# Performance work log

Hardware: AMD Instinct MI355X
Metric: run time of the kernel (lower is better)

The kernel has to match this reference:

```python
import jax, jax.numpy as jnp
import numpy as np

V, L, H, D = 2048, 16, 8, 64   # vocab, max_chars, n_head, word_vec_d
B = 8192                        # number of words in batch (rows of char_code)
NW_TOTAL = 8192                 # len(word_code)
N_NAMES = 2048                  # total names (4 words each)
N_GROUPS = 8                    # groups of names (256 each)
PAD = 0
TEMP = D ** 0.5
LN_EPS = 1e-5


def make_pos():
    freq = D // 2
    inv = 1.0 / np.power(10000.0, np.arange(freq) / freq)
    ph = np.outer(np.arange(L), inv)
    return jnp.asarray(np.hstack([np.cos(ph), np.sin(ph)]).astype(np.float32))


def setup_inputs() -> dict:
    key = jax.random.key(0)
    ks = jax.random.split(key, 8)
    char_emb = jax.random.normal(ks[0], (V, D), jnp.float32) * 0.02
    char_emb = char_emb.at[PAD].set(0.0)  # padding_idx row
    Wc = jax.random.normal(ks[1], (D, 3 * H * D), jnp.float32) * 0.02
    bc = jnp.zeros((3 * H * D,), jnp.float32)
    Wp = jax.random.normal(ks[2], (D, 3 * H * D), jnp.float32) * 0.02
    bp = jnp.zeros((3 * H * D,), jnp.float32)
    gamma = jnp.ones((D,), jnp.float32)
    beta = jnp.zeros((D,), jnp.float32)
    W1 = jax.random.normal(ks[3], (H, 16), jnp.float32) * 0.1
    b1 = jnp.zeros((16,), jnp.float32)
    W2 = jax.random.normal(ks[4], (16, 8), jnp.float32) * 0.1
    b2 = jnp.zeros((8,), jnp.float32)
    char_code = jax.random.randint(ks[5], (B, L), 1, V)
    char_code = char_code.at[::4, -2:].set(PAD)  # some padded tails
    word_code = jax.random.randint(ks[6], (NW_TOTAL,), 0, B)
    n_words = np.full((N_NAMES,), NW_TOTAL // N_NAMES, dtype=np.int64)
    n_names = np.full((N_GROUPS,), N_NAMES // N_GROUPS, dtype=np.int64)
    return {"char_emb": char_emb, "Wc": Wc, "bc": bc, "Wp": Wp, "bp": bp,
            "gamma": gamma, "beta": beta, "W1": W1, "b1": b1, "W2": W2, "b2": b2,
            "char_code": char_code, "word_code": word_code,
            "n_words": n_words, "n_names": n_names}


def reference(char_emb, Wc, bc, Wp, bp, gamma, beta, W1, b1, W2, b2,
              char_code, word_code, n_words, n_names):
    pos = make_pos()
    # ComputeQKV: linear d -> 3*H*d, reshape [N,3,H,D]
    cqkv = (char_emb @ Wc + bc).reshape(V, 3, H, D)
    cq, ck, cv = cqkv[:, 0], cqkv[:, 1], cqkv[:, 2]        # [V,H,D]
    pqkv = (pos @ Wp + bp).reshape(L, 3, H, D)
    pq, pk, pv = pqkv[:, 0], pqkv[:, 1], pqkv[:, 2]        # [L,H,D]
    # precomputed score tables
    char_qk = jnp.einsum('xhd,yhd->hxy', cq, ck).at[:, :, PAD].set(-1e9)  # [H,V,V]
    pos_qk = jnp.einsum('xhd,yhd->hxy', pq, pk)                            # [H,L,L]
    # char_q@pos_k + (pos_q@char_k)^T summed over the first dim of char_pos_qk
    cp = jnp.einsum('vhd,lhd->hvl', cq, pk) + jnp.einsum('lhd,vhd->hvl', pq, ck)  # [H,V,L]
    code = char_code                                        # [B,L]
    # gather-assembled scores, no [H,B*L,V] intermediate
    sim = (char_qk[:, code[:, :, None], code[:, None, :]]   # [H,B,L,L]
           + cp[:, code]
           + pos_qk[:, None]) / TEMP
    attn = jax.nn.softmax(sim, axis=-1)                     # [H,B,L,L] (dropout=0)
    v = jnp.transpose(cv[code], (2, 0, 1, 3)) + pv.transpose(1, 0, 2)[:, None]  # [H,B,L,D]
    out = jnp.einsum('hbij,hbjd->bihd', attn, v)            # [B,L,H,D]
    mu = out.mean(-1, keepdims=True)
    var = out.var(-1, keepdims=True)
    out = (out - mu) / jnp.sqrt(var + LN_EPS) * gamma + beta  # LayerNorm(D)
    char_ft = jnp.transpose(out, (0, 2, 1, 3))              # [B,H,L,D]
    mask = (code != PAD)
    pooled = jnp.einsum('bl,bhld->bhd', mask.astype(out.dtype), char_ft) \
             / mask.sum(-1)[:, None, None]                  # masked mean over chars
    x = jnp.transpose(pooled, (0, 2, 1))                    # [B,D,H]
    x = jax.nn.relu(x @ W1 + b1) @ W2 + b2                  # MLP over head dim -> [B,D,8]
    word_ft = x.reshape(B, -1)[word_code]                   # [NW_TOTAL, D*8]
    nw = np.asarray(n_words)
    seg = jnp.asarray(np.repeat(np.arange(nw.size), nw))
    name_ft = jax.ops.segment_sum(word_ft, seg, num_segments=nw.size) \
              / jnp.asarray(nw, word_ft.dtype)[:, None]     # ragged mean -> [N_NAMES, D*8]
    splits = np.cumsum(np.asarray(n_names))[:-1]
    return tuple(jnp.split(name_ft, splits, axis=0))
```

## Files before the change

### kernel.cpp

```cpp
#include <hip/hip_runtime.h>
#include <hip/hip_bf16.h>
#include <math.h>

typedef __attribute__((ext_vector_type(8))) short bfrag;
typedef __attribute__((ext_vector_type(4))) float ffrag;
typedef __attribute__((ext_vector_type(4))) float f4v;

#define C3 1536
#define PS 24

__device__ __forceinline__ unsigned short f2bf(float f) {
    unsigned u = __float_as_uint(f);
    return (unsigned short)((u + 0x7FFFu + ((u >> 16) & 1u)) >> 16);
}
__device__ __forceinline__ float bf2f(unsigned short s) {
    return __uint_as_float(((unsigned)s) << 16);
}

__device__ __forceinline__ float row16_sum(float x) {
    int v;
    v = __builtin_amdgcn_update_dpp(0, __float_as_int(x), 0xB1, 0xF, 0xF, true);
    x += __int_as_float(v);
    v = __builtin_amdgcn_update_dpp(0, __float_as_int(x), 0x4E, 0xF, 0xF, true);
    x += __int_as_float(v);
    v = __builtin_amdgcn_update_dpp(0, __float_as_int(x), 0x124, 0xF, 0xF, true);
    x += __int_as_float(v);
    v = __builtin_amdgcn_update_dpp(0, __float_as_int(x), 0x128, 0xF, 0xF, true);
    x += __int_as_float(v);
    return x;
}

__global__ __launch_bounds__(256) void precompute_kernel(
    const float* __restrict__ char_emb, const float* __restrict__ Wc, const float* __restrict__ bc,
    const float* __restrict__ Wp, const float* __restrict__ bp,
    unsigned short* __restrict__ cqkv, float* __restrict__ pqkv,
    unsigned short* __restrict__ pbf)
{
    const int b = blockIdx.x;
    const int t = threadIdx.x;
    if (b < 1536) {
        const int mt = b / 6;
        const int nt = b - mt * 6;
        const int m0 = mt * 8;
        const int c = nt * 256 + t;
        const float qs = (c < 512) ? 0.125f : 1.f;
        const float bias = bc[c];
        float acc[8];
        #pragma unroll
        for (int r = 0; r < 8; ++r) acc[r] = bias;
        #pragma unroll 16
        for (int dd = 0; dd < 64; ++dd) {
            const float wv = Wc[dd * C3 + c];
            #pragma unroll
            for (int r = 0; r < 8; ++r)
                acc[r] = fmaf(char_emb[(m0 + r) * 64 + dd], wv, acc[r]);
        }
        #pragma unroll
        for (int r = 0; r < 8; ++r)
            cqkv[(size_t)(m0 + r) * C3 + c] = f2bf(acc[r] * qs);
    } else {
        const int l = b - 1536;
        __shared__ float spos[64];
        if (t < 64) {
            const int f = t & 31;
            const float inv = exp2f(-(float)f * 0.41524101186092034f);
            const float ph = (float)l * inv;
            spos[t] = (t < 32) ? cosf(ph) : sinf(ph);
        }
        __syncthreads();
        #pragma unroll
        for (int cc = 0; cc < 6; ++cc) {
            const int c = t + cc * 256;
            float acc = bp[c];
            #pragma unroll
            for (int dd = 0; dd < 64; ++dd)
                acc = fmaf(spos[dd], Wp[dd * C3 + c], acc);
            pqkv[l * C3 + c] = acc;
            if (c < 1024) {
                const float qs = (c < 512) ? 0.125f : 1.f;
                pbf[(c >> 6) * 1024 + l * 64 + (c & 63)] = f2bf(acc * qs);
            }
        }
    }
}

__global__ __launch_bounds__(256) void vprime_kernel(
    const unsigned short* __restrict__ cqkv, const float* __restrict__ pqkv,
    unsigned short* __restrict__ vtab)
{
    const int c = blockIdx.x;
    const int t = threadIdx.x;
    const int hd8 = t & 63;
    const int l0 = t >> 6;
    const bfrag cv = *(const bfrag*)(cqkv + (size_t)c * C3 + 1024 + hd8 * 8);
    #pragma unroll
    for (int li = 0; li < 4; ++li) {
        const int l = l0 + li * 4;
        const f4v pa = *(const f4v*)(pqkv + l * C3 + 1024 + hd8 * 8);
        const f4v pb = *(const f4v*)(pqkv + l * C3 + 1024 + hd8 * 8 + 4);
        bfrag o;
        #pragma unroll
        for (int j = 0; j < 8; ++j)
            o[j] = (short)f2bf(bf2f((unsigned short)cv[j]) + ((j < 4) ? pa[j] : pb[j - 4]));
        *(bfrag*)(vtab + ((size_t)c * 16 + l) * 512 + hd8 * 8) = o;
    }
}

__global__ __launch_bounds__(256, 8) void attn_kernel(
    const unsigned short* __restrict__ cqkv, const unsigned short* __restrict__ pbf,
    const unsigned short* __restrict__ vtab, const int* __restrict__ char_code,
    const float* __restrict__ gamma, const float* __restrict__ beta,
    float* __restrict__ pooled)
{
    __shared__ __attribute__((aligned(16))) unsigned short sVt[4 * 1024];
    __shared__ __attribute__((aligned(16))) unsigned short sP[4 * 16 * PS];

    const int t = threadIdx.x;
    const int lane = t & 63;
    const int wid = t >> 6;
    const int gw = blockIdx.x * 4 + wid;
    const int w = gw >> 3;
    const int h = gw & 7;
    const int quad = lane >> 4;
    const int n = lane & 15;

    const int code = char_code[w * 16 + n];
    const bool kvalid = (code != 0);
    const unsigned long long msk = __ballot(kvalid);
    const int nv = __popcll(msk & 0xFFFFull);

    float gam[4], bet[4];
    #pragma unroll
    for (int dt = 0; dt < 4; ++dt) {
        gam[dt] = gamma[dt * 16 + n];
        bet[dt] = beta[dt * 16 + n];
    }

    unsigned short* vt = sVt + wid * 1024;
    #pragma unroll
    for (int cc = 0; cc < 2; ++cc) {
        const int d8 = quad + cc * 4;
        const bfrag vb = *(const bfrag*)(vtab + ((size_t)code * 16 + n) * 512 + h * 64 + d8 * 8);
        #pragma unroll
        for (int j = 0; j < 8; ++j) {
            const int d = d8 * 8 + j;
            const int e = ((d >> 4) * 2 + (n >> 3)) * 128
                        + ((d & 15) ^ ((n >> 3) << 2)) * 8 + (n & 7);
            vt[e] = (unsigned short)vb[j];
        }
    }

    ffrag accS = {0.f, 0.f, 0.f, 0.f};
    {
        const unsigned short* cbase = cqkv + (size_t)code * C3 + h * 64;
        const unsigned short* pq = pbf + h * 1024 + n * 64;
        const unsigned short* pk = pbf + (8 + h) * 1024 + n * 64;
        #pragma unroll
        for (int cc = 0; cc < 2; ++cc) {
            const int off = quad * 8 + cc * 32;
            const bfrag cqF = *(const bfrag*)(cbase + off);
            const bfrag ckF = *(const bfrag*)(cbase + 512 + off);
            const bfrag pqF = *(const bfrag*)(pq + off);
            const bfrag pkF = *(const bfrag*)(pk + off);
            accS = __builtin_amdgcn_mfma_f32_16x16x32_bf16(cqF, ckF, accS, 0, 0, 0);
            accS = __builtin_amdgcn_mfma_f32_16x16x32_bf16(cqF, pkF, accS, 0, 0, 0);
            accS = __builtin_amdgcn_mfma_f32_16x16x32_bf16(pqF, pkF, accS, 0, 0, 0);
            accS = __builtin_amdgcn_mfma_f32_16x16x32_bf16(ckF, pqF, accS, 0, 0, 0);
        }
    }

    float pr[4], sm[4];
    #pragma unroll
    for (int r = 0; r < 4; ++r) {
        pr[r] = kvalid ? __expf(accS[r]) : 0.f;
        sm[r] = row16_sum(pr[r]);
    }
    unsigned short* pt = sP + wid * 16 * PS;
    #pragma unroll
    for (int r = 0; r < 4; ++r)
        pt[(quad * 4 + r) * PS + n] = f2bf(pr[r]);

    bfrag ap;
    #pragma unroll
    for (int j = 0; j < 8; ++j) ap[j] = 0;
    if (quad < 2) ap = *(const bfrag*)(pt + n * PS + quad * 8);
    const int q2 = quad & 1;
    ffrag accO[4];
    #pragma unroll
    for (int dt = 0; dt < 4; ++dt) { ffrag z = {0.f,0.f,0.f,0.f}; accO[dt] = z; }
    #pragma unroll
    for (int dt = 0; dt < 4; ++dt) {
        const bfrag bv = *(const bfrag*)(vt + (dt * 2 + q2) * 128 + (n ^ (q2 << 2)) * 8);
        accO[dt] = __builtin_amdgcn_mfma_f32_16x16x32_bf16(ap, bv, accO[dt], 0, 0, 0);
    }

    float ps1[4], ps2[4];
    #pragma unroll
    for (int r = 0; r < 4; ++r) {
        ps1[r] = accO[0][r] + accO[1][r] + accO[2][r] + accO[3][r];
        ps2[r] = accO[0][r]*accO[0][r] + accO[1][r]*accO[1][r]
               + accO[2][r]*accO[2][r] + accO[3][r]*accO[3][r];
        ps1[r] = row16_sum(ps1[r]);
        ps2[r] = row16_sum(ps2[r]);
    }
    float pool[4] = {0.f, 0.f, 0.f, 0.f};
    #pragma unroll
    for (int r = 0; r < 4; ++r) {
        const float mu   = ps1[r] * 0.015625f;
        const float var  = fmaxf(ps2[r] * 0.015625f - mu * mu, 0.f);
        const float rstd = rsqrtf(var + sm[r] * sm[r] * 1e-5f);
        const float iv = ((msk >> (quad * 4 + r)) & 1ull) ? 1.f : 0.f;
        #pragma unroll
        for (int dt = 0; dt < 4; ++dt)
            pool[dt] += iv * fmaf((accO[dt][r] - mu) * rstd, gam[dt], bet[dt]);
    }
    #pragma unroll
    for (int xm = 16; xm <= 32; xm <<= 1) {
        #pragma unroll
        for (int dt = 0; dt < 4; ++dt) pool[dt] += __shfl_xor(pool[dt], xm);
    }
    if (quad == 0) {
        const float invnv = 1.f / (float)nv;
        f4v o;
        #pragma unroll
        for (int dt = 0; dt < 4; ++dt) o[dt] = pool[dt] * invnv;
        *(f4v*)(pooled + (size_t)w * 512 + h * 64 + n * 4) = o;
    }
}

__global__ __launch_bounds__(128) void mlp_avg_kernel(
    const float* __restrict__ pooled, const int* __restrict__ word_code,
    const int* __restrict__ n_words,
    const float* __restrict__ W1, const float* __restrict__ b1,
    const float* __restrict__ W2, const float* __restrict__ b2,
    float* __restrict__ out)
{
    __shared__ float sPool[512];
    __shared__ float sHid[64 * 17];
    __shared__ float sWb[280];
    __shared__ int sred[128];
    const int nm = blockIdx.x;
    const int t = threadIdx.x;
    sWb[t] = W1[t];
    sWb[144 + t] = W2[t];
    if (t < 16) sWb[128 + t] = b1[t];
    if (t < 8)  sWb[272 + t] = b2[t];

    int part = 0;
    for (int i = t; i < nm; i += 128) part += n_words[i];
    sred[t] = part;
    __syncthreads();
    for (int s = 64; s > 0; s >>= 1) {
        if (t < s) sred[t] += sred[t + s];
        __syncthreads();
    }
    const int off = sred[0];
    const int cnt = n_words[nm];

    const int d = t & 63, o4 = (t >> 6) * 4;
    const int dmap = (d & 15) * 4 + (d >> 4);
    float xacc[4] = {0.f, 0.f, 0.f, 0.f};

    for (int r = 0; r < cnt; ++r) {
        const int wc = word_code[off + r];
        __syncthreads();
        *(f4v*)(sPool + t * 4) = *(const f4v*)(pooled + (size_t)wc * 512 + t * 4);
        __syncthreads();
        if (t < 64) {
            float pl[8];
            #pragma unroll
            for (int hh = 0; hh < 8; ++hh) pl[hh] = sPool[hh * 64 + dmap];
            #pragma unroll
            for (int c = 0; c < 16; ++c) {
                float hs = sWb[128 + c];
                #pragma unroll
                for (int hh = 0; hh < 8; ++hh) hs = fmaf(pl[hh], sWb[hh * 16 + c], hs);
                sHid[t * 17 + c] = fmaxf(hs, 0.f);
            }
        }
        __syncthreads();
        #pragma unroll
        for (int c = 0; c < 16; ++c) {
            const float hc = sHid[d * 17 + c];
            #pragma unroll
            for (int oo = 0; oo < 4; ++oo)
                xacc[oo] = fmaf(hc, sWb[144 + c * 8 + o4 + oo], xacc[oo]);
        }
    }
    const float inv = 1.f / (float)cnt;
    f4v res;
    #pragma unroll
    for (int oo = 0; oo < 4; ++oo) res[oo] = xacc[oo] * inv + sWb[272 + o4 + oo];
    *(f4v*)(out + (size_t)nm * 512 + d * 8 + o4) = res;
}

extern "C" void kernel_launch(void* const* d_in, const int* in_sizes, int n_in,
                              void* d_out, int out_size, void* d_ws, size_t ws_size,
                              hipStream_t stream) {
    (void)in_sizes; (void)n_in; (void)out_size; (void)ws_size;
    const float* char_emb = (const float*)d_in[0];
    const float* Wc    = (const float*)d_in[1];
    const float* bc    = (const float*)d_in[2];
    const float* Wp    = (const float*)d_in[3];
    const float* bp    = (const float*)d_in[4];
    const float* gamma = (const float*)d_in[5];
    const float* beta  = (const float*)d_in[6];
    const float* W1    = (const float*)d_in[7];
    const float* b1    = (const float*)d_in[8];
    const float* W2    = (const float*)d_in[9];
    const float* b2    = (const float*)d_in[10];
    const int* char_code = (const int*)d_in[11];
    const int* word_code = (const int*)d_in[12];
    const int* n_words   = (const int*)d_in[13];

    char* ws = (char*)d_ws;
    unsigned short* cqkv = (unsigned short*)ws;
    float* pqkv = (float*)(ws + 6291456);
    unsigned short* pbf  = (unsigned short*)(ws + 6389760);
    unsigned short* vtab = (unsigned short*)(ws + 6422528);
    float* pooled = (float*)(ws + 39976960);
    float* out = (float*)d_out;

    precompute_kernel<<<1552, 256, 0, stream>>>(char_emb, Wc, bc, Wp, bp, cqkv, pqkv, pbf);
    vprime_kernel<<<2048, 256, 0, stream>>>(cqkv, pqkv, vtab);
    attn_kernel<<<16384, 256, 0, stream>>>(cqkv, pbf, vtab, char_code, gamma, beta, pooled);
    mlp_avg_kernel<<<2048, 128, 0, stream>>>(pooled, word_code, n_words,
                                             W1, b1, W2, b2, out);
}
```

Measured before the change: 204.5 us.

## Precompute positional QK scores and fold softmax row sums into an MFMA

The position-only q·k term, which is the same for every word, is now computed once per head in an extra vprime block and loaded as the initial MFMA accumulator. This removes one MFMA per chunk in the attention kernel. The softmax row sum is taken from an MFMA against a ones fragment instead of DPP row reductions. The position-projection precompute is also split across more blocks, and gamma/beta are packed into a table read with vector loads. The changes add small tables and extra blocks, and the row sum now comes from bf16-rounded probabilities.

```diff
diff --git a/kernel.cpp b/kernel.cpp
--- a/kernel.cpp
+++ b/kernel.cpp
@@ -33,8 +33,9 @@
 __global__ __launch_bounds__(256) void precompute_kernel(
     const float* __restrict__ char_emb, const float* __restrict__ Wc, const float* __restrict__ bc,
     const float* __restrict__ Wp, const float* __restrict__ bp,
+    const float* __restrict__ gamma, const float* __restrict__ beta,
     unsigned short* __restrict__ cqkv, float* __restrict__ pqkv,
-    unsigned short* __restrict__ pbf)
+    unsigned short* __restrict__ pbf, float* __restrict__ gbtab)
 {
     const int b = blockIdx.x;
     const int t = threadIdx.x;
@@ -59,7 +60,16 @@
         for (int r = 0; r < 8; ++r)
             cqkv[(size_t)(m0 + r) * C3 + c] = f2bf(acc[r] * qs);
     } else {
-        const int l = b - 1536;
+        const int e = b - 1536;
+        const int l = e / 6;
+        const int cc = e - l * 6;
+        if (b == 1536 && t < 64) {
+            #pragma unroll
+            for (int dt = 0; dt < 4; ++dt) {
+                gbtab[t * 8 + dt]     = gamma[dt * 16 + t];
+                gbtab[t * 8 + 4 + dt] = beta[dt * 16 + t];
+            }
+        }
         __shared__ float spos[64];
         if (t < 64) {
             const int f = t & 31;
@@ -68,28 +78,42 @@
             spos[t] = (t < 32) ? cosf(ph) : sinf(ph);
         }
         __syncthreads();
-        #pragma unroll
-        for (int cc = 0; cc < 6; ++cc) {
-            const int c = t + cc * 256;
-            float acc = bp[c];
-            #pragma unroll
-            for (int dd = 0; dd < 64; ++dd)
-                acc = fmaf(spos[dd], Wp[dd * C3 + c], acc);
-            pqkv[l * C3 + c] = acc;
-            if (c < 1024) {
-                const float qs = (c < 512) ? 0.125f : 1.f;
-                pbf[(c >> 6) * 1024 + l * 64 + (c & 63)] = f2bf(acc * qs);
-            }
+        const int c = t + cc * 256;
+        float acc = bp[c];
+        #pragma unroll
+        for (int dd = 0; dd < 64; ++dd)
+            acc = fmaf(spos[dd], Wp[dd * C3 + c], acc);
+        pqkv[l * C3 + c] = acc;
+        if (c < 1024) {
+            const float qs = (c < 512) ? 0.125f : 1.f;
+            pbf[(c >> 6) * 1024 + l * 64 + (c & 63)] = f2bf(acc * qs);
         }
     }
 }
 
 __global__ __launch_bounds__(256) void vprime_kernel(
     const unsigned short* __restrict__ cqkv, const float* __restrict__ pqkv,
-    unsigned short* __restrict__ vtab)
+    unsigned short* __restrict__ vtab, float* __restrict__ posqk)
 {
     const int c = blockIdx.x;
     const int t = threadIdx.x;
+    if (c >= 2048) {
+        const int h = c - 2048;
+        const int i = t >> 4, j = t & 15;
+        const f4v* qa = (const f4v*)(pqkv + i * C3 + h * 64);
+        const f4v* kb = (const f4v*)(pqkv + j * C3 + 512 + h * 64);
+        float acc = 0.f;
+        #pragma unroll
+        for (int x = 0; x < 16; ++x) {
+            const f4v a = qa[x], bb = kb[x];
+            acc = fmaf(a[0], bb[0], acc);
+            acc = fmaf(a[1], bb[1], acc);
+            acc = fmaf(a[2], bb[2], acc);
+            acc = fmaf(a[3], bb[3], acc);
+        }
+        posqk[h * 256 + (i >> 2) * 64 + j * 4 + (i & 3)] = acc * 0.125f;
+        return;
+    }
     const int hd8 = t & 63;
     const int l0 = t >> 6;
     const bfrag cv = *(const bfrag*)(cqkv + (size_t)c * C3 + 1024 + hd8 * 8);
@@ -109,7 +133,7 @@
 __global__ __launch_bounds__(256, 8) void attn_kernel(
     const unsigned short* __restrict__ cqkv, const unsigned short* __restrict__ pbf,
     const unsigned short* __restrict__ vtab, const int* __restrict__ char_code,
-    const float* __restrict__ gamma, const float* __restrict__ beta,
+    const float* __restrict__ posqk, const float* __restrict__ gbtab,
     float* __restrict__ pooled)
 {
     __shared__ __attribute__((aligned(16))) unsigned short sVt[4 * 1024];
@@ -129,12 +153,8 @@
     const unsigned long long msk = __ballot(kvalid);
     const int nv = __popcll(msk & 0xFFFFull);
 
-    float gam[4], bet[4];
-    #pragma unroll
-    for (int dt = 0; dt < 4; ++dt) {
-        gam[dt] = gamma[dt * 16 + n];
-        bet[dt] = beta[dt * 16 + n];
-    }
+    const f4v g4 = *(const f4v*)(gbtab + n * 8);
+    const f4v b4 = *(const f4v*)(gbtab + n * 8 + 4);
 
     unsigned short* vt = sVt + wid * 1024;
     #pragma unroll
@@ -150,7 +170,7 @@
         }
     }
 
-    ffrag accS = {0.f, 0.f, 0.f, 0.f};
+    ffrag accS = *(const ffrag*)(posqk + h * 256 + quad * 64 + n * 4);
     {
         const unsigned short* cbase = cqkv + (size_t)code * C3 + h * 64;
         const unsigned short* pq = pbf + h * 1024 + n * 64;
@@ -164,21 +184,16 @@
             const bfrag pkF = *(const bfrag*)(pk + off);
             accS = __builtin_amdgcn_mfma_f32_16x16x32_bf16(cqF, ckF, accS, 0, 0, 0);
             accS = __builtin_amdgcn_mfma_f32_16x16x32_bf16(cqF, pkF, accS, 0, 0, 0);
-            accS = __builtin_amdgcn_mfma_f32_16x16x32_bf16(pqF, pkF, accS, 0, 0, 0);
             accS = __builtin_amdgcn_mfma_f32_16x16x32_bf16(ckF, pqF, accS, 0, 0, 0);
         }
     }
 
-    float pr[4], sm[4];
+    unsigned short* pt = sP + wid * 16 * PS;
     #pragma unroll
     for (int r = 0; r < 4; ++r) {
-        pr[r] = kvalid ? __expf(accS[r]) : 0.f;
-        sm[r] = row16_sum(pr[r]);
-    }
-    unsigned short* pt = sP + wid * 16 * PS;
-    #pragma unroll
-    for (int r = 0; r < 4; ++r)
-        pt[(quad * 4 + r) * PS + n] = f2bf(pr[r]);
+        const float pr = kvalid ? __expf(accS[r]) : 0.f;
+        pt[(quad * 4 + r) * PS + n] = f2bf(pr);
+    }
 
     bfrag ap;
     #pragma unroll
@@ -193,6 +208,11 @@
         const bfrag bv = *(const bfrag*)(vt + (dt * 2 + q2) * 128 + (n ^ (q2 << 2)) * 8);
         accO[dt] = __builtin_amdgcn_mfma_f32_16x16x32_bf16(ap, bv, accO[dt], 0, 0, 0);
     }
+    bfrag onesf;
+    #pragma unroll
+    for (int j = 0; j < 8; ++j) onesf[j] = (short)0x3F80;
+    ffrag accE = {0.f, 0.f, 0.f, 0.f};
+    accE = __builtin_amdgcn_mfma_f32_16x16x32_bf16(ap, onesf, accE, 0, 0, 0);
 
     float ps1[4], ps2[4];
     #pragma unroll
@@ -208,11 +228,11 @@
     for (int r = 0; r < 4; ++r) {
         const float mu   = ps1[r] * 0.015625f;
         const float var  = fmaxf(ps2[r] * 0.015625f - mu * mu, 0.f);
-        const float rstd = rsqrtf(var + sm[r] * sm[r] * 1e-5f);
+        const float rstd = rsqrtf(var + accE[r] * accE[r] * 1e-5f);
         const float iv = ((msk >> (quad * 4 + r)) & 1ull) ? 1.f : 0.f;
         #pragma unroll
         for (int dt = 0; dt < 4; ++dt)
-            pool[dt] += iv * fmaf((accO[dt][r] - mu) * rstd, gam[dt], bet[dt]);
+            pool[dt] += iv * fmaf((accO[dt][r] - mu) * rstd, g4[dt], b4[dt]);
     }
     #pragma unroll
     for (int xm = 16; xm <= 32; xm <<= 1) {
@@ -319,11 +339,14 @@
     unsigned short* pbf  = (unsigned short*)(ws + 6389760);
     unsigned short* vtab = (unsigned short*)(ws + 6422528);
     float* pooled = (float*)(ws + 39976960);
+    float* posqk  = (float*)(ws + 56754176);
+    float* gbtab  = (float*)(ws + 56762368);
     float* out = (float*)d_out;
 
-    precompute_kernel<<<1552, 256, 0, stream>>>(char_emb, Wc, bc, Wp, bp, cqkv, pqkv, pbf);
-    vprime_kernel<<<2048, 256, 0, stream>>>(cqkv, pqkv, vtab);
-    attn_kernel<<<16384, 256, 0, stream>>>(cqkv, pbf, vtab, char_code, gamma, beta, pooled);
+    precompute_kernel<<<1632, 256, 0, stream>>>(char_emb, Wc, bc, Wp, bp, gamma, beta,
+                                                cqkv, pqkv, pbf, gbtab);
+    vprime_kernel<<<2056, 256, 0, stream>>>(cqkv, pqkv, vtab, posqk);
+    attn_kernel<<<16384, 256, 0, stream>>>(cqkv, pbf, vtab, char_code, posqk, gbtab, pooled);
     mlp_avg_kernel<<<2048, 128, 0, stream>>>(pooled, word_code, n_words,
                                              W1, b1, W2, b2, out);
 }
```

Result: no change. 205.1 us (+0.3%).
